# Kernel optimization log

Hardware: AMD Instinct MI355X
Metric: run time of the kernel (lower is better)

## Reference

```python
import jax, jax.numpy as jnp
import numpy as np

EPS_F = 1e-6   # epsilon_F global in original repo
GAMMA = 0.8
K = 5
BN_EPS = 1e-5
M = 128
N = 100000
E = 1600000
MY = 10

def setup_inputs() -> dict:
    key = jax.random.key(0)
    ks = jax.random.split(key, 6)
    X = jax.random.normal(ks[0], (M, N), dtype=jnp.float32)
    # xavier_uniform for F: limit = sqrt(6/(m+m))
    lim = float(np.sqrt(6.0 / (M + M)))
    F_mat = jax.random.uniform(ks[1], (M, M), dtype=jnp.float32, minval=-lim, maxval=lim)
    B = (1.0 / np.sqrt(M)) * jax.random.normal(ks[2], (MY, M), dtype=jnp.float32)
    bn_weight = jnp.ones((M,), dtype=jnp.float32)
    bn_bias = jnp.zeros((M,), dtype=jnp.float32)
    edge_val = jax.random.uniform(ks[3], (E,), dtype=jnp.float32)
    edge_row = jax.random.randint(ks[4], (E,), 0, N, dtype=jnp.int64 if jax.config.jax_enable_x64 else jnp.int32)
    edge_col = jax.random.randint(ks[5], (E,), 0, N, dtype=jnp.int64 if jax.config.jax_enable_x64 else jnp.int32)
    return {"X": X, "F_mat": F_mat, "B": B, "bn_weight": bn_weight,
            "bn_bias": bn_bias, "edge_val": edge_val,
            "edge_row": edge_row, "edge_col": edge_col}

def reference(X, F_mat, B, bn_weight, bn_bias, edge_val, edge_row, edge_col):
    n = X.shape[1]
    # normalized Gram matrix g(F) = F^T F / (||F^T F||_fro + eps)
    FF = F_mat.T @ F_mat                       # [m, m]
    G = FF / (jnp.linalg.norm(FF) + EPS_F)
    X_first = X                                # [m, n]

    def step(Xc, _):
        Y = Xc.T                               # [n, m]
        # SpMM: (S_t @ Y)[r] += val * Y[c]
        SY = jax.ops.segment_sum(edge_val[:, None] * Y[edge_col], edge_row,
                                 num_segments=n)   # [n, m]
        Xn = GAMMA * (G @ SY.T) + X_first          # [m, n]
        return Xn, None

    Xk, _ = jax.lax.scan(step, X, None, length=K)
    out = Xk.T                                 # [n, m]
    # BatchNorm1d over feature dim (training-mode batch stats); dropout omitted (eval)
    mu = out.mean(axis=0)
    var = out.var(axis=0)
    out = (out - mu) * jax.lax.rsqrt(var + BN_EPS) * bn_weight + bn_bias
    return out @ B.T                           # [n, m_y]
```

## Files before the change

kernel.cpp:

```cpp
#include <hip/hip_runtime.h>
#include <math.h>

#define MDIM 128
#define MY 10
#define GAMMA 0.8f
#define KITER 5

__device__ __forceinline__ float bf2f(unsigned short h) {
    return __uint_as_float(((unsigned int)h) << 16);
}
__device__ __forceinline__ unsigned short f2bf(float f) {
    unsigned int u = __float_as_uint(f);
    u += 0x7fffu + ((u >> 16) & 1u);
    return (unsigned short)(u >> 16);
}

__global__ void k_transpose(const float* __restrict__ X, float* __restrict__ Y0,
                            unsigned short* __restrict__ Y0h, int n) {
    __shared__ float tile[32][33];
    int r0 = blockIdx.x * 32;
    int f0 = blockIdx.y * 32;
    int tx = threadIdx.x, ty = threadIdx.y;
    #pragma unroll
    for (int i = 0; i < 32; i += 8) {
        tile[ty + i][tx] = X[(size_t)(f0 + ty + i) * n + (r0 + tx)];
    }
    __syncthreads();
    #pragma unroll
    for (int i = 0; i < 32; i += 8) {
        float v = tile[tx][ty + i];
        Y0[(size_t)(r0 + ty + i) * MDIM + (f0 + tx)] = v;
        Y0h[(size_t)(r0 + ty + i) * MDIM + (f0 + tx)] = f2bf(v);
    }
}

__global__ void k_gram(const float* __restrict__ F, float* __restrict__ FF,
                       float* __restrict__ normAcc) {
    int i = blockIdx.x, j = threadIdx.x;
    float acc = 0.f;
    for (int k = 0; k < MDIM; ++k)
        acc = fmaf(F[k * MDIM + i], F[k * MDIM + j], acc);
    FF[i * MDIM + j] = acc;
    __shared__ float red[MDIM];
    red[j] = acc * acc;
    __syncthreads();
    for (int s = 64; s > 0; s >>= 1) {
        if (j < s) red[j] += red[j + s];
        __syncthreads();
    }
    if (j == 0) atomicAdd(normAcc, red[0]);
}

__global__ void k_gnorm(const float* __restrict__ FF, const float* __restrict__ normAcc,
                        float* __restrict__ G) {
    int idx = blockIdx.x * 256 + threadIdx.x;
    float s = GAMMA / (sqrtf(*normAcc) + 1e-6f);
    G[idx] = FF[idx] * s;
}

__global__ void k_hist(const int* __restrict__ erow, int* __restrict__ cnt, int E) {
    int e = blockIdx.x * 256 + threadIdx.x;
    if (e < E) atomicAdd(&cnt[erow[e]], 1);
}

__global__ void k_scan1(const int* __restrict__ cnt, int* __restrict__ blockSums, int n) {
    int tid = threadIdx.x;
    int base = blockIdx.x * 1024 + tid * 4;
    int s = 0;
    if (base + 3 < n) {
        int4 v = *(const int4*)&cnt[base];
        s = v.x + v.y + v.z + v.w;
    } else {
        for (int i = 0; i < 4; ++i)
            if (base + i < n) s += cnt[base + i];
    }
    __shared__ int red[256];
    red[tid] = s;
    __syncthreads();
    for (int st = 128; st > 0; st >>= 1) {
        if (tid < st) red[tid] += red[tid + st];
        __syncthreads();
    }
    if (tid == 0) blockSums[blockIdx.x] = red[0];
}

__global__ void k_scan2(int* __restrict__ blockSums, int* __restrict__ row_off,
                        int nb, int n) {
    __shared__ int s[256];
    int tid = threadIdx.x;
    int v = (tid < nb) ? blockSums[tid] : 0;
    s[tid] = v;
    __syncthreads();
    for (int off = 1; off < 256; off <<= 1) {
        int t = (tid >= off) ? s[tid - off] : 0;
        __syncthreads();
        s[tid] += t;
        __syncthreads();
    }
    if (tid < nb) blockSums[tid] = s[tid] - v;
    if (tid == 0) row_off[n] = s[255];
}

__global__ void k_scan3(const int* __restrict__ cnt, const int* __restrict__ blockOff,
                        int* __restrict__ row_off, int n) {
    int tid = threadIdx.x;
    int base = blockIdx.x * 1024 + tid * 4;
    int v[4];
    #pragma unroll
    for (int i = 0; i < 4; ++i) v[i] = (base + i < n) ? cnt[base + i] : 0;
    int local = v[0] + v[1] + v[2] + v[3];
    __shared__ int s[256];
    s[tid] = local;
    __syncthreads();
    for (int off = 1; off < 256; off <<= 1) {
        int t = (tid >= off) ? s[tid - off] : 0;
        __syncthreads();
        s[tid] += t;
        __syncthreads();
    }
    int excl = s[tid] - local + blockOff[blockIdx.x];
    #pragma unroll
    for (int i = 0; i < 4; ++i) {
        if (base + i < n) { row_off[base + i] = excl; excl += v[i]; }
    }
}

__global__ void k_scatter(const int* __restrict__ erow, const int* __restrict__ ecol,
                          const float* __restrict__ eval_, int* __restrict__ cursor,
                          int2* __restrict__ csr_cv, int E) {
    int e = blockIdx.x * 256 + threadIdx.x;
    if (e < E) {
        int r = erow[e];
        int pos = atomicAdd(&cursor[r], 1);
        csr_cv[pos] = make_int2(ecol[e], __float_as_int(eval_[e]));
    }
}

__global__ void __launch_bounds__(256, 8) k_fused(const unsigned short* __restrict__ Yh,
                                                  const int* __restrict__ row_off,
                                                  const int2* __restrict__ csr_cv,
                                                  const float* __restrict__ G,
                                                  const float* __restrict__ Y0,
                                                  float* __restrict__ Yout,
                                                  unsigned short* __restrict__ Yhout,
                                                  float* __restrict__ stats,
                                                  int writeH, int writeF, int n) {
    __shared__ float sSY[32 * MDIM];
    int tid = threadIdx.x;
    int ty = tid >> 5;
    int tx = tid & 31;
    int rbase = blockIdx.x * 32;

    for (int i = 0; i < 4; ++i) {
        int rloc = ty * 4 + i;
        int e0 = row_off[rbase + rloc];
        int e1 = row_off[rbase + rloc + 1];
        float4 a = make_float4(0.f, 0.f, 0.f, 0.f);
        int e = e0;
        for (; e + 4 <= e1; e += 4) {
            int2 p0 = csr_cv[e + 0];
            int2 p1 = csr_cv[e + 1];
            int2 p2 = csr_cv[e + 2];
            int2 p3 = csr_cv[e + 3];
            ushort4 h0 = *(const ushort4*)&Yh[(size_t)p0.x * MDIM + tx * 4];
            ushort4 h1 = *(const ushort4*)&Yh[(size_t)p1.x * MDIM + tx * 4];
            ushort4 h2 = *(const ushort4*)&Yh[(size_t)p2.x * MDIM + tx * 4];
            ushort4 h3 = *(const ushort4*)&Yh[(size_t)p3.x * MDIM + tx * 4];
            float v0 = __int_as_float(p0.y);
            float v1 = __int_as_float(p1.y);
            float v2 = __int_as_float(p2.y);
            float v3 = __int_as_float(p3.y);
            a.x = fmaf(v0, bf2f(h0.x), a.x);
            a.y = fmaf(v0, bf2f(h0.y), a.y);
            a.z = fmaf(v0, bf2f(h0.z), a.z);
            a.w = fmaf(v0, bf2f(h0.w), a.w);
            a.x = fmaf(v1, bf2f(h1.x), a.x);
            a.y = fmaf(v1, bf2f(h1.y), a.y);
            a.z = fmaf(v1, bf2f(h1.z), a.z);
            a.w = fmaf(v1, bf2f(h1.w), a.w);
            a.x = fmaf(v2, bf2f(h2.x), a.x);
            a.y = fmaf(v2, bf2f(h2.y), a.y);
            a.z = fmaf(v2, bf2f(h2.z), a.z);
            a.w = fmaf(v2, bf2f(h2.w), a.w);
            a.x = fmaf(v3, bf2f(h3.x), a.x);
            a.y = fmaf(v3, bf2f(h3.y), a.y);
            a.z = fmaf(v3, bf2f(h3.z), a.z);
            a.w = fmaf(v3, bf2f(h3.w), a.w);
        }
        for (; e < e1; ++e) {
            int2 p = csr_cv[e];
            float v = __int_as_float(p.y);
            ushort4 h = *(const ushort4*)&Yh[(size_t)p.x * MDIM + tx * 4];
            a.x = fmaf(v, bf2f(h.x), a.x);
            a.y = fmaf(v, bf2f(h.y), a.y);
            a.z = fmaf(v, bf2f(h.z), a.z);
            a.w = fmaf(v, bf2f(h.w), a.w);
        }
        *(float4*)&sSY[rloc * MDIM + tx * 4] = a;
    }

    size_t r0 = (size_t)rbase + ty * 4;
    int f0 = tx * 4;
    float4 acc[4];
    #pragma unroll
    for (int i = 0; i < 4; ++i) acc[i] = make_float4(0.f, 0.f, 0.f, 0.f);

    for (int j = 0; j < MDIM; j += 4) {
        float4 g0 = *(const float4*)&G[(j + 0) * MDIM + f0];
        float4 g1 = *(const float4*)&G[(j + 1) * MDIM + f0];
        float4 g2 = *(const float4*)&G[(j + 2) * MDIM + f0];
        float4 g3 = *(const float4*)&G[(j + 3) * MDIM + f0];
        #pragma unroll
        for (int i = 0; i < 4; ++i) {
            float4 sr = *(const float4*)&sSY[(ty * 4 + i) * MDIM + j];
            acc[i].x = fmaf(sr.x, g0.x, acc[i].x);
            acc[i].y = fmaf(sr.x, g0.y, acc[i].y);
            acc[i].z = fmaf(sr.x, g0.z, acc[i].z);
            acc[i].w = fmaf(sr.x, g0.w, acc[i].w);
            acc[i].x = fmaf(sr.y, g1.x, acc[i].x);
            acc[i].y = fmaf(sr.y, g1.y, acc[i].y);
            acc[i].z = fmaf(sr.y, g1.z, acc[i].z);
            acc[i].w = fmaf(sr.y, g1.w, acc[i].w);
            acc[i].x = fmaf(sr.z, g2.x, acc[i].x);
            acc[i].y = fmaf(sr.z, g2.y, acc[i].y);
            acc[i].z = fmaf(sr.z, g2.z, acc[i].z);
            acc[i].w = fmaf(sr.z, g2.w, acc[i].w);
            acc[i].x = fmaf(sr.w, g3.x, acc[i].x);
            acc[i].y = fmaf(sr.w, g3.y, acc[i].y);
            acc[i].z = fmaf(sr.w, g3.z, acc[i].z);
            acc[i].w = fmaf(sr.w, g3.w, acc[i].w);
        }
    }

    float4 bs = make_float4(0.f, 0.f, 0.f, 0.f);
    float4 bq = make_float4(0.f, 0.f, 0.f, 0.f);
    #pragma unroll
    for (int i = 0; i < 4; ++i) {
        float4 y0 = *(const float4*)&Y0[(r0 + i) * MDIM + f0];
        float4 o;
        o.x = acc[i].x + y0.x;
        o.y = acc[i].y + y0.y;
        o.z = acc[i].z + y0.z;
        o.w = acc[i].w + y0.w;
        if (writeF) {
            *(float4*)&Yout[(r0 + i) * MDIM + f0] = o;
            bs.x += o.x; bs.y += o.y; bs.z += o.z; bs.w += o.w;
            bq.x = fmaf(o.x, o.x, bq.x);
            bq.y = fmaf(o.y, o.y, bq.y);
            bq.z = fmaf(o.z, o.z, bq.z);
            bq.w = fmaf(o.w, o.w, bq.w);
        }
        if (writeH) {
            ushort4 h;
            h.x = f2bf(o.x);
            h.y = f2bf(o.y);
            h.z = f2bf(o.z);
            h.w = f2bf(o.w);
            *(ushort4*)&Yhout[(r0 + i) * MDIM + f0] = h;
        }
    }

    if (writeF) {
        __syncthreads();
        *(float4*)&sSY[ty * MDIM + f0] = bs;
        *(float4*)&sSY[8 * MDIM + ty * MDIM + f0] = bq;
        __syncthreads();
        if (tid < MDIM) {
            float a = 0.f, b = 0.f;
            #pragma unroll
            for (int t = 0; t < 8; ++t) {
                a += sSY[t * MDIM + tid];
                b += sSY[8 * MDIM + t * MDIM + tid];
            }
            atomicAdd(&stats[tid], a);
            atomicAdd(&stats[MDIM + tid], b);
        }
    }
}

__global__ void k_finalize(const float* __restrict__ stats, const float* __restrict__ B,
                           const float* __restrict__ bnw, const float* __restrict__ bnb,
                           float* __restrict__ Bs, float* __restrict__ cvec, int n) {
    int f = threadIdx.x;
    float inv_n = 1.f / (float)n;
    float mu = stats[f] * inv_n;
    float var = stats[MDIM + f] * inv_n - mu * mu;
    float rs = rsqrtf(var + 1e-5f);
    float sw = rs * bnw[f];
    float cv = bnb[f] - mu * sw;
    __shared__ float red[MDIM];
    for (int o = 0; o < MY; ++o) {
        float b = B[o * MDIM + f];
        Bs[o * MDIM + f] = b * sw;
        red[f] = b * cv;
        __syncthreads();
        for (int s = 64; s > 0; s >>= 1) {
            if (f < s) red[f] += red[f + s];
            __syncthreads();
        }
        if (f == 0) cvec[o] = red[0];
        __syncthreads();
    }
}

__global__ void __launch_bounds__(256) k_project(const float* __restrict__ Y,
                                                 const float* __restrict__ Bs,
                                                 const float* __restrict__ cvec,
                                                 float* __restrict__ out, int n) {
    __shared__ float yt[16 * 129];
    __shared__ float sB[MY * 129];
    __shared__ float sc[MY];
    int tid = threadIdx.x;
    size_t rbase = (size_t)blockIdx.x * 16;
    for (int idx = tid; idx < 16 * MDIM; idx += 256) {
        int r = idx >> 7, f = idx & 127;
        yt[r * 129 + f] = Y[(rbase + r) * MDIM + f];
    }
    for (int idx = tid; idx < MY * MDIM; idx += 256) {
        int o = idx >> 7, f = idx & 127;
        sB[o * 129 + f] = Bs[idx];
    }
    if (tid < MY) sc[tid] = cvec[tid];
    __syncthreads();
    if (tid < 16 * MY) {
        int r = tid / MY, o = tid % MY;
        float acc = sc[o];
        for (int f = 0; f < MDIM; ++f)
            acc = fmaf(yt[r * 129 + f], sB[o * 129 + f], acc);
        out[(rbase + r) * MY + o] = acc;
    }
}

extern "C" void kernel_launch(void* const* d_in, const int* in_sizes, int n_in,
                              void* d_out, int out_size, void* d_ws, size_t ws_size,
                              hipStream_t stream) {
    const float* X    = (const float*)d_in[0];
    const float* F    = (const float*)d_in[1];
    const float* B    = (const float*)d_in[2];
    const float* bnw  = (const float*)d_in[3];
    const float* bnb  = (const float*)d_in[4];
    const float* ev   = (const float*)d_in[5];
    const int*   erow = (const int*)d_in[6];
    const int*   ecol = (const int*)d_in[7];
    float* out = (float*)d_out;
    const int n = in_sizes[0] / MDIM;
    const int E = in_sizes[5];

    char* w = (char*)d_ws;
    size_t off = 0;
    auto carve = [&](size_t bytes) -> void* {
        void* p = w + off;
        off += (bytes + 255) & ~(size_t)255;
        return p;
    };
    float*          Y0    = (float*)carve((size_t)n * MDIM * 4);
    float*          Ycur  = (float*)carve((size_t)n * MDIM * 4);
    unsigned short* Yh_a  = (unsigned short*)carve((size_t)n * MDIM * 2);
    unsigned short* Yh_b  = (unsigned short*)carve((size_t)n * MDIM * 2);
    float* FF        = (float*)carve(MDIM * MDIM * 4);
    float* G         = (float*)carve(MDIM * MDIM * 4);
    int2*  csr_cv    = (int2*)carve((size_t)E * 8);
    int*   row_off   = (int*)carve((size_t)(n + 1) * 4);
    int*   cursor    = (int*)carve((size_t)n * 4);
    int*   cnt       = (int*)carve((size_t)n * 4);
    int*   blockSums = (int*)carve(1024 * 4);
    float* normAcc   = (float*)carve(4);
    float* stats     = (float*)carve(2 * MDIM * 4);
    float* Bs        = (float*)carve(MY * MDIM * 4);
    float* cvec      = (float*)carve(MY * 4);
    (void)ws_size;

    hipMemsetAsync(cnt, 0, (size_t)n * 4, stream);
    hipMemsetAsync(normAcc, 0, 4, stream);
    hipMemsetAsync(stats, 0, 2 * MDIM * 4, stream);

    k_transpose<<<dim3(n / 32, MDIM / 32), dim3(32, 8), 0, stream>>>(X, Y0, Yh_a, n);
    k_gram<<<MDIM, MDIM, 0, stream>>>(F, FF, normAcc);
    k_gnorm<<<MDIM * MDIM / 256, 256, 0, stream>>>(FF, normAcc, G);

    const int nb = (n + 1023) / 1024;
    k_hist<<<(E + 255) / 256, 256, 0, stream>>>(erow, cnt, E);
    k_scan1<<<nb, 256, 0, stream>>>(cnt, blockSums, n);
    k_scan2<<<1, 256, 0, stream>>>(blockSums, row_off, nb, n);
    k_scan3<<<nb, 256, 0, stream>>>(cnt, blockSums, row_off, n);
    hipMemcpyAsync(cursor, row_off, (size_t)n * 4, hipMemcpyDeviceToDevice, stream);
    k_scatter<<<(E + 255) / 256, 256, 0, stream>>>(erow, ecol, ev, cursor, csr_cv, E);

    for (int k = 0; k < KITER; ++k) {
        const unsigned short* hin = (k & 1) ? Yh_b : Yh_a;
        unsigned short*       hout = (k & 1) ? Yh_a : Yh_b;
        int writeH = (k < KITER - 1) ? 1 : 0;
        int writeF = (k == KITER - 1) ? 1 : 0;
        k_fused<<<n / 32, 256, 0, stream>>>(hin, row_off, csr_cv, G, Y0, Ycur, hout,
                                            stats, writeH, writeF, n);
    }

    k_finalize<<<1, MDIM, 0, stream>>>(stats, B, bnw, bnb, Bs, cvec, n);
    k_project<<<n / 16, 256, 0, stream>>>(Ycur, Bs, cvec, out, n);
}
```

Before: 920.4 us.

## Multi-pass row-range CSR scatter, bf16 residual, pre-shifted column offsets, 8-way unroll

The CSR scatter now runs in 8 passes, each handling one row range, so atomics and writes stay localized and cache-friendly, at the cost of re-reading the edge arrays 8 times. Column indices are stored pre-shifted into byte offsets, which removes the index multiply in the gather. The gather loop is unrolled 8-wide for more memory-level parallelism. Non-final iterations read a bf16 copy of the initial residual instead of fp32, halving that traffic but adding rounding error to intermediate iterations.

```diff
diff --git a/kernel.cpp b/kernel.cpp
--- a/kernel.cpp
+++ b/kernel.cpp
@@ -5,6 +5,7 @@
 #define MY 10
 #define GAMMA 0.8f
 #define KITER 5
+#define NPASS 8
 
 __device__ __forceinline__ float bf2f(unsigned short h) {
     return __uint_as_float(((unsigned int)h) << 16);
@@ -16,7 +17,8 @@
 }
 
 __global__ void k_transpose(const float* __restrict__ X, float* __restrict__ Y0,
-                            unsigned short* __restrict__ Y0h, int n) {
+                            unsigned short* __restrict__ Y0h,
+                            unsigned short* __restrict__ Yh0, int n) {
     __shared__ float tile[32][33];
     int r0 = blockIdx.x * 32;
     int f0 = blockIdx.y * 32;
@@ -29,8 +31,10 @@
     #pragma unroll
     for (int i = 0; i < 32; i += 8) {
         float v = tile[tx][ty + i];
+        unsigned short h = f2bf(v);
         Y0[(size_t)(r0 + ty + i) * MDIM + (f0 + tx)] = v;
-        Y0h[(size_t)(r0 + ty + i) * MDIM + (f0 + tx)] = f2bf(v);
+        Y0h[(size_t)(r0 + ty + i) * MDIM + (f0 + tx)] = h;
+        Yh0[(size_t)(r0 + ty + i) * MDIM + (f0 + tx)] = h;
     }
 }
 
@@ -127,12 +131,14 @@
 
 __global__ void k_scatter(const int* __restrict__ erow, const int* __restrict__ ecol,
                           const float* __restrict__ eval_, int* __restrict__ cursor,
-                          int2* __restrict__ csr_cv, int E) {
+                          int2* __restrict__ csr_cv, int E, int rlo, int rhi) {
     int e = blockIdx.x * 256 + threadIdx.x;
     if (e < E) {
         int r = erow[e];
-        int pos = atomicAdd(&cursor[r], 1);
-        csr_cv[pos] = make_int2(ecol[e], __float_as_int(eval_[e]));
+        if (r >= rlo && r < rhi) {
+            int pos = atomicAdd(&cursor[r], 1);
+            csr_cv[pos] = make_int2(ecol[e] << 8, __float_as_int(eval_[e]));
+        }
     }
 }
 
@@ -141,6 +147,7 @@
                                                   const int2* __restrict__ csr_cv,
                                                   const float* __restrict__ G,
                                                   const float* __restrict__ Y0,
+                                                  const unsigned short* __restrict__ Y0h,
                                                   float* __restrict__ Yout,
                                                   unsigned short* __restrict__ Yhout,
                                                   float* __restrict__ stats,
@@ -150,6 +157,8 @@
     int ty = tid >> 5;
     int tx = tid & 31;
     int rbase = blockIdx.x * 32;
+    const char* yb = (const char*)Yh;
+    int lbo = tx * 8;
 
     for (int i = 0; i < 4; ++i) {
         int rloc = ty * 4 + i;
@@ -157,15 +166,73 @@
         int e1 = row_off[rbase + rloc + 1];
         float4 a = make_float4(0.f, 0.f, 0.f, 0.f);
         int e = e0;
+        for (; e + 8 <= e1; e += 8) {
+            int2 p0 = csr_cv[e + 0];
+            int2 p1 = csr_cv[e + 1];
+            int2 p2 = csr_cv[e + 2];
+            int2 p3 = csr_cv[e + 3];
+            int2 p4 = csr_cv[e + 4];
+            int2 p5 = csr_cv[e + 5];
+            int2 p6 = csr_cv[e + 6];
+            int2 p7 = csr_cv[e + 7];
+            ushort4 h0 = *(const ushort4*)(yb + (size_t)(p0.x + lbo));
+            ushort4 h1 = *(const ushort4*)(yb + (size_t)(p1.x + lbo));
+            ushort4 h2 = *(const ushort4*)(yb + (size_t)(p2.x + lbo));
+            ushort4 h3 = *(const ushort4*)(yb + (size_t)(p3.x + lbo));
+            ushort4 h4 = *(const ushort4*)(yb + (size_t)(p4.x + lbo));
+            ushort4 h5 = *(const ushort4*)(yb + (size_t)(p5.x + lbo));
+            ushort4 h6 = *(const ushort4*)(yb + (size_t)(p6.x + lbo));
+            ushort4 h7 = *(const ushort4*)(yb + (size_t)(p7.x + lbo));
+            float v0 = __int_as_float(p0.y);
+            float v1 = __int_as_float(p1.y);
+            float v2 = __int_as_float(p2.y);
+            float v3 = __int_as_float(p3.y);
+            float v4 = __int_as_float(p4.y);
+            float v5 = __int_as_float(p5.y);
+            float v6 = __int_as_float(p6.y);
+            float v7 = __int_as_float(p7.y);
+            a.x = fmaf(v0, bf2f(h0.x), a.x);
+            a.y = fmaf(v0, bf2f(h0.y), a.y);
+            a.z = fmaf(v0, bf2f(h0.z), a.z);
+            a.w = fmaf(v0, bf2f(h0.w), a.w);
+            a.x = fmaf(v1, bf2f(h1.x), a.x);
+            a.y = fmaf(v1, bf2f(h1.y), a.y);
+            a.z = fmaf(v1, bf2f(h1.z), a.z);
+            a.w = fmaf(v1, bf2f(h1.w), a.w);
+            a.x = fmaf(v2, bf2f(h2.x), a.x);
+            a.y = fmaf(v2, bf2f(h2.y), a.y);
+            a.z = fmaf(v2, bf2f(h2.z), a.z);
+            a.w = fmaf(v2, bf2f(h2.w), a.w);
+            a.x = fmaf(v3, bf2f(h3.x), a.x);
+            a.y = fmaf(v3, bf2f(h3.y), a.y);
+            a.z = fmaf(v3, bf2f(h3.z), a.z);
+            a.w = fmaf(v3, bf2f(h3.w), a.w);
+            a.x = fmaf(v4, bf2f(h4.x), a.x);
+            a.y = fmaf(v4, bf2f(h4.y), a.y);
+            a.z = fmaf(v4, bf2f(h4.z), a.z);
+            a.w = fmaf(v4, bf2f(h4.w), a.w);
+            a.x = fmaf(v5, bf2f(h5.x), a.x);
+            a.y = fmaf(v5, bf2f(h5.y), a.y);
+            a.z = fmaf(v5, bf2f(h5.z), a.z);
+            a.w = fmaf(v5, bf2f(h5.w), a.w);
+            a.x = fmaf(v6, bf2f(h6.x), a.x);
+            a.y = fmaf(v6, bf2f(h6.y), a.y);
+            a.z = fmaf(v6, bf2f(h6.z), a.z);
+            a.w = fmaf(v6, bf2f(h6.w), a.w);
+            a.x = fmaf(v7, bf2f(h7.x), a.x);
+            a.y = fmaf(v7, bf2f(h7.y), a.y);
+            a.z = fmaf(v7, bf2f(h7.z), a.z);
+            a.w = fmaf(v7, bf2f(h7.w), a.w);
+        }
         for (; e + 4 <= e1; e += 4) {
             int2 p0 = csr_cv[e + 0];
             int2 p1 = csr_cv[e + 1];
             int2 p2 = csr_cv[e + 2];
             int2 p3 = csr_cv[e + 3];
-            ushort4 h0 = *(const ushort4*)&Yh[(size_t)p0.x * MDIM + tx * 4];
-            ushort4 h1 = *(const ushort4*)&Yh[(size_t)p1.x * MDIM + tx * 4];
-            ushort4 h2 = *(const ushort4*)&Yh[(size_t)p2.x * MDIM + tx * 4];
-            ushort4 h3 = *(const ushort4*)&Yh[(size_t)p3.x * MDIM + tx * 4];
+            ushort4 h0 = *(const ushort4*)(yb + (size_t)(p0.x + lbo));
+            ushort4 h1 = *(const ushort4*)(yb + (size_t)(p1.x + lbo));
+            ushort4 h2 = *(const ushort4*)(yb + (size_t)(p2.x + lbo));
+            ushort4 h3 = *(const ushort4*)(yb + (size_t)(p3.x + lbo));
             float v0 = __int_as_float(p0.y);
             float v1 = __int_as_float(p1.y);
             float v2 = __int_as_float(p2.y);
@@ -190,7 +257,7 @@
         for (; e < e1; ++e) {
             int2 p = csr_cv[e];
             float v = __int_as_float(p.y);
-            ushort4 h = *(const ushort4*)&Yh[(size_t)p.x * MDIM + tx * 4];
+            ushort4 h = *(const ushort4*)(yb + (size_t)(p.x + lbo));
             a.x = fmaf(v, bf2f(h.x), a.x);
             a.y = fmaf(v, bf2f(h.y), a.y);
             a.z = fmaf(v, bf2f(h.z), a.z);
@@ -236,7 +303,16 @@
     float4 bq = make_float4(0.f, 0.f, 0.f, 0.f);
     #pragma unroll
     for (int i = 0; i < 4; ++i) {
-        float4 y0 = *(const float4*)&Y0[(r0 + i) * MDIM + f0];
+        float4 y0;
+        if (writeF) {
+            y0 = *(const float4*)&Y0[(r0 + i) * MDIM + f0];
+        } else {
+            ushort4 t = *(const ushort4*)&Y0h[(r0 + i) * MDIM + f0];
+            y0.x = bf2f(t.x);
+            y0.y = bf2f(t.y);
+            y0.z = bf2f(t.z);
+            y0.w = bf2f(t.w);
+        }
         float4 o;
         o.x = acc[i].x + y0.x;
         o.y = acc[i].y + y0.y;
@@ -355,6 +431,7 @@
     };
     float*          Y0    = (float*)carve((size_t)n * MDIM * 4);
     float*          Ycur  = (float*)carve((size_t)n * MDIM * 4);
+    unsigned short* Y0h   = (unsigned short*)carve((size_t)n * MDIM * 2);
     unsigned short* Yh_a  = (unsigned short*)carve((size_t)n * MDIM * 2);
     unsigned short* Yh_b  = (unsigned short*)carve((size_t)n * MDIM * 2);
     float* FF        = (float*)carve(MDIM * MDIM * 4);
@@ -374,7 +451,7 @@
     hipMemsetAsync(normAcc, 0, 4, stream);
     hipMemsetAsync(stats, 0, 2 * MDIM * 4, stream);
 
-    k_transpose<<<dim3(n / 32, MDIM / 32), dim3(32, 8), 0, stream>>>(X, Y0, Yh_a, n);
+    k_transpose<<<dim3(n / 32, MDIM / 32), dim3(32, 8), 0, stream>>>(X, Y0, Y0h, Yh_a, n);
     k_gram<<<MDIM, MDIM, 0, stream>>>(F, FF, normAcc);
     k_gnorm<<<MDIM * MDIM / 256, 256, 0, stream>>>(FF, normAcc, G);
 
@@ -384,14 +461,21 @@
     k_scan2<<<1, 256, 0, stream>>>(blockSums, row_off, nb, n);
     k_scan3<<<nb, 256, 0, stream>>>(cnt, blockSums, row_off, n);
     hipMemcpyAsync(cursor, row_off, (size_t)n * 4, hipMemcpyDeviceToDevice, stream);
-    k_scatter<<<(E + 255) / 256, 256, 0, stream>>>(erow, ecol, ev, cursor, csr_cv, E);
+    const int rstep = (n + NPASS - 1) / NPASS;
+    for (int p = 0; p < NPASS; ++p) {
+        int rlo = p * rstep;
+        int rhi = rlo + rstep;
+        if (rhi > n) rhi = n;
+        k_scatter<<<(E + 255) / 256, 256, 0, stream>>>(erow, ecol, ev, cursor,
+                                                       csr_cv, E, rlo, rhi);
+    }
 
     for (int k = 0; k < KITER; ++k) {
         const unsigned short* hin = (k & 1) ? Yh_b : Yh_a;
         unsigned short*       hout = (k & 1) ? Yh_a : Yh_b;
         int writeH = (k < KITER - 1) ? 1 : 0;
         int writeF = (k == KITER - 1) ? 1 : 0;
-        k_fused<<<n / 32, 256, 0, stream>>>(hin, row_off, csr_cv, G, Y0, Ycur, hout,
+        k_fused<<<n / 32, 256, 0, stream>>>(hin, row_off, csr_cv, G, Y0, Y0h, Ycur, hout,
                                             stats, writeH, writeF, n);
     }
 
```

New measurement: 929.5 us. No clear change (+1.0%).
